# Kernel tuning notes

Hardware: AMD Instinct MI355X
Metric: run time of the kernel (lower is better)

## Reference

```python
import jax, jax.numpy as jnp
import numpy as np

D_EMBED = 1024


def setup_inputs() -> dict:
    key = jax.random.key(0)
    ks = jax.random.split(key, 8)
    B, S, D = 8, 2048, D_EMBED
    scale = 1.0 / np.sqrt(D)
    return {
        "embeddings": jax.random.normal(ks[0], (B, S, D), dtype=jnp.float32),
        "mask": jnp.zeros((B, S, S), dtype=jnp.float32),
        "Wq": jax.random.normal(ks[1], (D, D), dtype=jnp.float32) * scale,
        "bq": jax.random.normal(ks[2], (D,), dtype=jnp.float32) * 0.02,
        "Wk": jax.random.normal(ks[3], (D, D), dtype=jnp.float32) * scale,
        "bk": jax.random.normal(ks[4], (D,), dtype=jnp.float32) * 0.02,
        "Wv": jax.random.normal(ks[5], (D, D), dtype=jnp.float32) * scale,
        "bv": jax.random.normal(ks[6], (D,), dtype=jnp.float32) * 0.02,
    }


def reference(embeddings, mask, Wq, bq, Wk, bk, Wv, bv):
    # torch Linear: y = x @ W.T + b
    q = jnp.einsum('bsd,ed->bse', embeddings, Wq) + bq
    k = jnp.einsum('bsd,ed->bse', embeddings, Wk) + bk
    v = jnp.einsum('bsd,ed->bse', embeddings, Wv) + bv
    scores = jnp.einsum('bqd,bkd->bqk', q, k)
    # NOTE: faithful to source — mask added BEFORE scaling by 1/sqrt(d)
    scores = (scores + mask) * (1.0 / jnp.sqrt(jnp.float32(q.shape[-1])))
    attn = jax.nn.softmax(scores, axis=-1)
    return jnp.einsum('bqk,bkd->bqd', attn, v)
```

## Files before the change

### kernel.cpp

```cpp
#include <hip/hip_runtime.h>


#define B_SZ 8
#define SEQ  2048
#define DIM  1024
#define MROWS (B_SZ * SEQ)

typedef unsigned short u16;
typedef short short8 __attribute__((ext_vector_type(8)));
typedef unsigned short u16x4 __attribute__((ext_vector_type(4)));
typedef float f32x4 __attribute__((ext_vector_type(4)));

__device__ __forceinline__ u16 f2h(float x) {
  _Float16 h = (_Float16)x;
  union { _Float16 f; u16 u; } c; c.f = h; return c.u;
}
__device__ __forceinline__ float h2f(u16 u) {
  union { _Float16 f; u16 u; } c; c.u = u; return (float)c.f;
}

__device__ __forceinline__ int xcd_swz(int x, int nwg) {
  return (x & 7) * (nwg >> 3) + (x >> 3);
}

__device__ __forceinline__ void gload_lds16(const u16* g, u16* l) {
  __builtin_amdgcn_global_load_lds(
      (__attribute__((address_space(1))) void*)(g),
      (__attribute__((address_space(3))) void*)(l), 16, 0, 0);
}

__device__ __forceinline__ f32x4 mfma_f16(short8 a, short8 b, f32x4 c) {
  asm("v_mfma_f32_16x16x32_f16 %0, %1, %2, %0" : "+v"(c) : "v"(a), "v"(b));
  return c;
}

__device__ __forceinline__ void gemm256_core(const u16* __restrict__ Ag,
                                             const u16* __restrict__ Bg,
                                             int NT, size_t lda, size_t ldb,
                                             u16* sm, f32x4 (&acc)[8][4]) {
  const int tid = threadIdx.x;
  const int lane = tid & 63;
  const int wid = tid >> 6;
  const int wm8 = (wid >> 2) << 3;
  const int wn4 = (wid & 3) << 2;

  u16* sA = sm;
  u16* sB = sm + 32768;

  const int bb = (lane << 4) ^ (((lane >> 5) & 1) << 5);
  const int rins = bb >> 6;
  const int cins = (bb & 63) >> 1;
  const int s0 = wid, s1 = 8 + wid, s2 = 16 + wid, s3 = 24 + wid;
  const size_t aoff0 = (size_t)((s0 >> 1) * 16 + rins) * lda + ((s0 & 1) * 32 + cins);
  const size_t aoff1 = (size_t)((s1 >> 1) * 16 + rins) * lda + ((s1 & 1) * 32 + cins);
  const size_t aoff2 = (size_t)((s2 >> 1) * 16 + rins) * lda + ((s2 & 1) * 32 + cins);
  const size_t aoff3 = (size_t)((s3 >> 1) * 16 + rins) * lda + ((s3 & 1) * 32 + cins);
  const size_t boff0 = (size_t)((s0 >> 1) * 16 + rins) * ldb + ((s0 & 1) * 32 + cins);
  const size_t boff1 = (size_t)((s1 >> 1) * 16 + rins) * ldb + ((s1 & 1) * 32 + cins);
  const size_t boff2 = (size_t)((s2 >> 1) * 16 + rins) * ldb + ((s2 & 1) * 32 + cins);
  const size_t boff3 = (size_t)((s3 >> 1) * 16 + rins) * ldb + ((s3 & 1) * 32 + cins);
  const int wid512 = wid << 9;

  const int lof = ((lane & 15) << 6) + ((lane >> 4) << 4);
  const int loe = (lof ^ (((lane >> 3) & 1) << 5)) >> 1;

#define ISSUE_A(j, nb, kt) \
  gload_lds16(Ag + aoff##j + (size_t)(kt) * 64, sA + (nb) * 16384 + (j) * 4096 + wid512)
#define ISSUE_B(j, nb, kt) \
  gload_lds16(Bg + boff##j + (size_t)(kt) * 64, sB + (nb) * 16384 + (j) * 4096 + wid512)

  ISSUE_B(0, 0, 0); ISSUE_B(1, 0, 0); ISSUE_B(2, 0, 0); ISSUE_B(3, 0, 0);
  ISSUE_A(0, 0, 0); ISSUE_A(2, 0, 0); ISSUE_A(1, 0, 0); ISSUE_A(3, 0, 0);

  int buf = 0;
  for (int kt = 0; kt < NT; ++kt) {
    const int nk = kt + 1;
    const bool pre = nk < NT;
    const int nb = buf ^ 1;
    asm volatile("s_waitcnt vmcnt(2)" ::: "memory");
    __builtin_amdgcn_s_barrier();
    asm volatile("" ::: "memory");
    const u16* bufA = sA + buf * 16384;
    const u16* bufB = sB + buf * 16384;
    short8 bf[4][2];
    short8 a0[2][2], a1[2][2];
#pragma unroll
    for (int n = 0; n < 4; ++n) {
      bf[n][0] = *(const short8*)(bufB + (wn4 + n) * 1024 + loe);
      bf[n][1] = *(const short8*)(bufB + (wn4 + n) * 1024 + 512 + loe);
    }
#pragma unroll
    for (int m = 0; m < 2; ++m) {
      a0[m][0] = *(const short8*)(bufA + (wm8 + m) * 1024 + loe);
      a0[m][1] = *(const short8*)(bufA + (wm8 + m) * 1024 + 512 + loe);
    }
    if (pre) { ISSUE_B(0, nb, nk); ISSUE_B(1, nb, nk); }
    __builtin_amdgcn_s_setprio(1);
#pragma unroll
    for (int m = 0; m < 2; ++m)
#pragma unroll
      for (int n = 0; n < 4; ++n) {
        acc[m][n] = mfma_f16(a0[m][0], bf[n][0], acc[m][n]);
        acc[m][n] = mfma_f16(a0[m][1], bf[n][1], acc[m][n]);
      }
    __builtin_amdgcn_s_setprio(0);
#pragma unroll
    for (int m = 0; m < 2; ++m) {
      a1[m][0] = *(const short8*)(bufA + (wm8 + 2 + m) * 1024 + loe);
      a1[m][1] = *(const short8*)(bufA + (wm8 + 2 + m) * 1024 + 512 + loe);
    }
    if (pre) { ISSUE_B(2, nb, nk); ISSUE_B(3, nb, nk); }
    __builtin_amdgcn_s_barrier();
    asm volatile("" ::: "memory");
    __builtin_amdgcn_s_setprio(1);
#pragma unroll
    for (int m = 0; m < 2; ++m)
#pragma unroll
      for (int n = 0; n < 4; ++n) {
        acc[2 + m][n] = mfma_f16(a1[m][0], bf[n][0], acc[2 + m][n]);
        acc[2 + m][n] = mfma_f16(a1[m][1], bf[n][1], acc[2 + m][n]);
      }
    __builtin_amdgcn_s_setprio(0);
    if (pre) {
      asm volatile("s_waitcnt vmcnt(4)" ::: "memory");
    } else {
      asm volatile("s_waitcnt vmcnt(0)" ::: "memory");
    }
    __builtin_amdgcn_s_barrier();
    asm volatile("" ::: "memory");
#pragma unroll
    for (int m = 0; m < 2; ++m) {
      a0[m][0] = *(const short8*)(bufA + (wm8 + 4 + m) * 1024 + loe);
      a0[m][1] = *(const short8*)(bufA + (wm8 + 4 + m) * 1024 + 512 + loe);
      a1[m][0] = *(const short8*)(bufA + (wm8 + 6 + m) * 1024 + loe);
      a1[m][1] = *(const short8*)(bufA + (wm8 + 6 + m) * 1024 + 512 + loe);
    }
    if (pre) { ISSUE_A(0, nb, nk); ISSUE_A(2, nb, nk); }
    __builtin_amdgcn_s_setprio(1);
#pragma unroll
    for (int m = 0; m < 2; ++m)
#pragma unroll
      for (int n = 0; n < 4; ++n) {
        acc[4 + m][n] = mfma_f16(a0[m][0], bf[n][0], acc[4 + m][n]);
        acc[4 + m][n] = mfma_f16(a0[m][1], bf[n][1], acc[4 + m][n]);
      }
    __builtin_amdgcn_s_setprio(0);
    if (pre) { ISSUE_A(1, nb, nk); ISSUE_A(3, nb, nk); }
    __builtin_amdgcn_s_barrier();
    asm volatile("" ::: "memory");
    __builtin_amdgcn_s_setprio(1);
#pragma unroll
    for (int m = 0; m < 2; ++m)
#pragma unroll
      for (int n = 0; n < 4; ++n) {
        acc[6 + m][n] = mfma_f16(a1[m][0], bf[n][0], acc[6 + m][n]);
        acc[6 + m][n] = mfma_f16(a1[m][1], bf[n][1], acc[6 + m][n]);
      }
    __builtin_amdgcn_s_setprio(0);
    buf ^= 1;
  }
  asm volatile("s_nop 7\n\ts_nop 7\n\ts_nop 7" ::);
#undef ISSUE_A
#undef ISSUE_B
}

__device__ __forceinline__ void gemm128_core(const u16* A, const u16* Bt, int K,
                                             int lda, int ldb, f32x4 (&acc)[4][4],
                                             u16* sA, u16* sB) {
  const int tid = threadIdx.x;
  const int lane = tid & 63;
  const int wid = tid >> 6;
  const int wr = wid >> 1;
  const int wc = wid & 1;
  const int srow = tid >> 2;
  const int scol = (tid & 3) << 3;
  const u16* ga0 = A + (size_t)srow * lda + scol;
  const u16* ga1 = A + (size_t)(srow + 64) * lda + scol;
  const u16* gb0 = Bt + (size_t)srow * ldb + scol;
  const u16* gb1 = Bt + (size_t)(srow + 64) * ldb + scol;
  u16* la0 = sA + (wid << 9);
  u16* la1 = sA + 2048 + (wid << 9);
  u16* lb0 = sB + (wid << 9);
  u16* lb1 = sB + 2048 + (wid << 9);
  const u16* pa = sA + (size_t)((wr << 6) + (lane & 15)) * 32 + ((lane >> 4) << 3);
  const u16* pb = sB + (size_t)((wc << 6) + (lane & 15)) * 32 + ((lane >> 4) << 3);
  const int ksteps = K >> 5;
  for (int kt = 0; kt < ksteps; ++kt) {
    gload_lds16(ga0, la0);
    gload_lds16(ga1, la1);
    gload_lds16(gb0, lb0);
    gload_lds16(gb1, lb1);
    ga0 += 32; ga1 += 32; gb0 += 32; gb1 += 32;
    __syncthreads();
    short8 a[4], b[4];
#pragma unroll
    for (int i = 0; i < 4; ++i) a[i] = *(const short8*)(pa + (i << 9));
#pragma unroll
    for (int i = 0; i < 4; ++i) b[i] = *(const short8*)(pb + (i << 9));
#pragma unroll
    for (int mi = 0; mi < 4; ++mi)
#pragma unroll
      for (int ni = 0; ni < 4; ++ni)
        acc[mi][ni] = mfma_f16(a[mi], b[ni], acc[mi][ni]);
    __syncthreads();
  }
  asm volatile("s_nop 7\n\ts_nop 7\n\ts_nop 7" ::);
}

__global__ __launch_bounds__(256) void prep_kernel(const float* __restrict__ emb,
                                                   const float* __restrict__ Wq,
                                                   const float* __restrict__ Wk,
                                                   const float* __restrict__ Wv,
                                                   const float* __restrict__ bq,
                                                   u16* __restrict__ emb16,
                                                   u16* __restrict__ WqT,
                                                   u16* __restrict__ WkT,
                                                   u16* __restrict__ Wv16,
                                                   float* __restrict__ w) {
  __shared__ float t[64][65];
  const int b = blockIdx.x;
  const int tid = threadIdx.x;
  if (b < 16384) {
    int i = b * 256 + tid;
    float4 v = ((const float4*)emb)[i];
    u16x4 o;
    o[0] = f2h(v.x); o[1] = f2h(v.y); o[2] = f2h(v.z); o[3] = f2h(v.w);
    ((u16x4*)emb16)[i] = o;
  } else if (b < 16896) {
    const int b2 = b - 16384;
    const float* src = (b2 >> 8) ? Wk : Wq;
    u16* dst = (b2 >> 8) ? WkT : WqT;
    const int rem = b2 & 255;
    const int r0 = (rem >> 4) * 64;
    const int c0 = (rem & 15) * 64;
    const int tr = tid >> 4;
    const int c4 = (tid & 15) << 2;
#pragma unroll
    for (int i = 0; i < 4; ++i) {
      float4 x = *(const float4*)(src + (size_t)(r0 + tr + 16 * i) * 1024 + c0 + c4);
      t[tr + 16 * i][c4 + 0] = x.x;
      t[tr + 16 * i][c4 + 1] = x.y;
      t[tr + 16 * i][c4 + 2] = x.z;
      t[tr + 16 * i][c4 + 3] = x.w;
    }
    __syncthreads();
#pragma unroll
    for (int i = 0; i < 4; ++i) {
      int dr = tr + 16 * i;
      u16x4 y;
      y[0] = f2h(t[c4 + 0][dr]);
      y[1] = f2h(t[c4 + 1][dr]);
      y[2] = f2h(t[c4 + 2][dr]);
      y[3] = f2h(t[c4 + 3][dr]);
      *(u16x4*)(dst + (size_t)(c0 + dr) * 1024 + r0 + c4) = y;
    }
  } else if (b < 17920) {
    int i = (b - 16896) * 256 + tid;
    float4 v = ((const float4*)Wv)[i];
    u16x4 o;
    o[0] = f2h(v.x); o[1] = f2h(v.y); o[2] = f2h(v.z); o[3] = f2h(v.w);
    ((u16x4*)Wv16)[i] = o;
  } else {
    const int wb = b - 17920;
    const int el = tid & 31;
    const int rg = tid >> 5;
    const int e = wb * 32 + el;
    float s = 0.f;
    const float* col = Wk + e;
#pragma unroll 4
    for (int r = rg * 128; r < rg * 128 + 128; ++r)
      s += col[(size_t)r * 1024] * bq[r];
    float* red = &t[0][0];
    red[rg * 32 + el] = s;
    __syncthreads();
    if (tid < 32) {
      float a = 0.f;
#pragma unroll
      for (int g = 0; g < 8; ++g) a += red[g * 32 + tid];
      w[wb * 32 + tid] = a * 0.03125f;
    }
  }
}

__global__ __launch_bounds__(256) void cmt_kernel(const u16* __restrict__ emb16,
                                                  const u16* __restrict__ WqT,
                                                  const u16* __restrict__ WkT,
                                                  const float* __restrict__ w,
                                                  float* __restrict__ c,
                                                  float* __restrict__ MtP) {
  __shared__ __align__(16) u16 smem[8192];
  const int b = blockIdx.x;
  const int tid = threadIdx.x;
  if (b < 4096) {
    float* sw = (float*)smem;
    for (int i = tid; i < 1024; i += 256) sw[i] = w[i];
    __syncthreads();
    const int wv = tid >> 6, lane = tid & 63;
    const int r = b * 4 + wv;
    const u16* row = emb16 + (size_t)r * 1024;
    float s = 0.f;
#pragma unroll
    for (int it = 0; it < 2; ++it) {
      int d = lane * 8 + it * 512;
      short8 v = *(const short8*)(row + d);
#pragma unroll
      for (int j = 0; j < 8; ++j) s += h2f((u16)v[j]) * sw[d + j];
    }
#pragma unroll
    for (int off = 1; off < 64; off <<= 1) s += __shfl_xor(s, off);
    if (lane == 0) c[r] = s;
  } else {
    const int b2 = b - 4096;
    const int tile = b2 >> 2;
    const int kc = b2 & 3;
    const int m0 = (tile >> 3) * 128;
    const int n0 = (tile & 7) * 128;
    f32x4 acc[4][4] = {};
    gemm128_core(WkT + (size_t)m0 * 1024 + kc * 256,
                 WqT + (size_t)n0 * 1024 + kc * 256, 256, 1024, 1024,
                 acc, smem, smem + 4096);
    const int lane = tid & 63, wid = tid >> 6;
    const int wr = wid >> 1, wc = wid & 1;
    float* plane = MtP + (size_t)kc * 1024 * 1024;
#pragma unroll
    for (int mi = 0; mi < 4; ++mi)
#pragma unroll
      for (int ni = 0; ni < 4; ++ni)
#pragma unroll
        for (int j = 0; j < 4; ++j) {
          int row = m0 + (wr << 6) + mi * 16 + ((lane >> 4) << 2) + j;
          int col = n0 + (wc << 6) + ni * 16 + (lane & 15);
          plane[(size_t)row * 1024 + col] = acc[mi][ni][j];
        }
  }
}

__global__ __launch_bounds__(256) void mtred_kernel(const float* __restrict__ MtP,
                                                    u16* __restrict__ Mt) {
  const size_t i = (size_t)blockIdx.x * 1024 + threadIdx.x * 4;
  float4 a = *(const float4*)(MtP + i);
  float4 b = *(const float4*)(MtP + 1048576 + i);
  float4 cc = *(const float4*)(MtP + 2097152 + i);
  float4 d = *(const float4*)(MtP + 3145728 + i);
  u16x4 o;
  o[0] = f2h((a.x + b.x + cc.x + d.x) * 0.03125f);
  o[1] = f2h((a.y + b.y + cc.y + d.y) * 0.03125f);
  o[2] = f2h((a.z + b.z + cc.z + d.z) * 0.03125f);
  o[3] = f2h((a.w + b.w + cc.w + d.w) * 0.03125f);
  *(u16x4*)(Mt + i) = o;
}

__global__ __launch_bounds__(512) void proj256_kernel(const u16* __restrict__ emb16,
                                                      const u16* __restrict__ Mt,
                                                      const u16* __restrict__ Wv16,
                                                      const float* __restrict__ bv,
                                                      u16* __restrict__ G,
                                                      u16* __restrict__ vT) {
  __shared__ __align__(16) u16 sm[65536];
  const int wg = xcd_swz(blockIdx.x, 512);
  const int lane = threadIdx.x & 63, wid = threadIdx.x >> 6;
  f32x4 acc[8][4] = {};
  if (wg < 256) {
    const int m0 = (wg >> 2) * 256;
    const int n0 = (wg & 3) * 256;
    gemm256_core(emb16 + (size_t)m0 * 1024, Mt + (size_t)n0 * 1024, 16, 1024, 1024,
                 sm, acc);
    const int rb = m0 + ((wid >> 2) << 7) + ((lane >> 4) << 2);
    const int cb = n0 + ((wid & 3) << 6) + (lane & 15);
#pragma unroll
    for (int m = 0; m < 8; ++m)
#pragma unroll
      for (int n = 0; n < 4; ++n)
#pragma unroll
        for (int j = 0; j < 4; ++j)
          G[(size_t)(rb + m * 16 + j) * 1024 + (cb + n * 16)] = f2h(acc[m][n][j]);
  } else {
    const int r = wg - 256;
    const int m0 = (r & 3) * 256;
    const int n0 = (r >> 2) * 256;
    gemm256_core(Wv16 + (size_t)m0 * 1024, emb16 + (size_t)n0 * 1024, 16, 1024, 1024,
                 sm, acc);
    const int rb = m0 + ((wid >> 2) << 7) + ((lane >> 4) << 2);
    const int cb = n0 + ((wid & 3) << 6) + (lane & 15);
#pragma unroll
    for (int m = 0; m < 8; ++m)
#pragma unroll
      for (int n = 0; n < 4; ++n)
#pragma unroll
        for (int j = 0; j < 4; ++j) {
          int d = rb + m * 16 + j;
          int kg = cb + n * 16;
          int bi = kg >> 11, s = kg & 2047;
          vT[((size_t)bi << 21) + ((size_t)d << 11) + s] = f2h(acc[m][n][j] + bv[d]);
        }
  }
}

__global__ __launch_bounds__(512) void scores256_kernel(const u16* __restrict__ G,
                                                        const u16* __restrict__ emb16,
                                                        const float* __restrict__ c,
                                                        u16* __restrict__ scH) {
  __shared__ __align__(16) u16 sm[65536];
  const int wg = xcd_swz(blockIdx.x, 512);
  const int b = wg >> 6;
  const int m0 = ((wg >> 3) & 7) * 256;
  const int n0 = (wg & 7) * 256;
  f32x4 acc[8][4] = {};
  gemm256_core(G + ((size_t)b * SEQ + m0) * DIM, emb16 + ((size_t)b * SEQ + n0) * DIM,
               16, DIM, DIM, sm, acc);
  const int lane = threadIdx.x & 63, wid = threadIdx.x >> 6;
  const int rb = m0 + ((wid >> 2) << 7) + ((lane >> 4) << 2);
  const int cb = n0 + ((wid & 3) << 6) + (lane & 15);
  float cn[4];
#pragma unroll
  for (int n = 0; n < 4; ++n) cn[n] = c[(size_t)b * SEQ + cb + n * 16];
#pragma unroll
  for (int m = 0; m < 8; ++m)
#pragma unroll
    for (int n = 0; n < 4; ++n)
#pragma unroll
      for (int j = 0; j < 4; ++j) {
        size_t idx = ((size_t)b * SEQ + rb + m * 16 + j) * SEQ + (cb + n * 16);
        scH[idx] = f2h(acc[m][n][j] + cn[n]);
      }
}

__global__ __launch_bounds__(256) void softmax_kernel(u16* __restrict__ scH,
                                                      const float* __restrict__ mask) {
  __shared__ float red[8];
  const size_t row = blockIdx.x;
  u16* rowp = scH + row * SEQ;
  const float* mrow = mask + row * SEQ;
  const int tid = threadIdx.x;
  short8 raw = *(const short8*)(rowp + tid * 8);
  float4 m0 = ((const float4*)mrow)[2 * tid];
  float4 m1 = ((const float4*)mrow)[2 * tid + 1];
  float mk[8] = {m0.x, m0.y, m0.z, m0.w, m1.x, m1.y, m1.z, m1.w};
  float f[8];
#pragma unroll
  for (int j = 0; j < 8; ++j) f[j] = h2f((u16)raw[j]) + mk[j] * 0.03125f;
  float mx = f[0];
#pragma unroll
  for (int j = 1; j < 8; ++j) mx = fmaxf(mx, f[j]);
#pragma unroll
  for (int off = 1; off < 64; off <<= 1) mx = fmaxf(mx, __shfl_xor(mx, off));
  const int wid = tid >> 6, lane = tid & 63;
  if (lane == 0) red[wid] = mx;
  __syncthreads();
  mx = fmaxf(fmaxf(red[0], red[1]), fmaxf(red[2], red[3]));
  float e[8];
  float s = 0.f;
#pragma unroll
  for (int j = 0; j < 8; ++j) {
    e[j] = __expf(f[j] - mx);
    s += e[j];
  }
#pragma unroll
  for (int off = 1; off < 64; off <<= 1) s += __shfl_xor(s, off);
  if (lane == 0) red[4 + wid] = s;
  __syncthreads();
  s = (red[4] + red[5]) + (red[6] + red[7]);
  const float inv = 1.f / s;
  short8 o;
#pragma unroll
  for (int j = 0; j < 8; ++j) o[j] = (short)f2h(e[j] * inv);
  *(short8*)(rowp + tid * 8) = o;
}

__global__ __launch_bounds__(512) void pv256_kernel(const u16* __restrict__ pr,
                                                    const u16* __restrict__ vt,
                                                    float* __restrict__ out) {
  __shared__ __align__(16) u16 sm[65536];
  const int wg = xcd_swz(blockIdx.x, 256);
  const int b = wg >> 5;
  const int m0 = ((wg >> 2) & 7) * 256;
  const int n0 = (wg & 3) * 256;
  f32x4 acc[8][4] = {};
  gemm256_core(pr + ((size_t)b * SEQ + m0) * SEQ, vt + ((size_t)b * DIM + n0) * SEQ,
               32, SEQ, SEQ, sm, acc);
  const int lane = threadIdx.x & 63, wid = threadIdx.x >> 6;
  const int rb = m0 + ((wid >> 2) << 7) + ((lane >> 4) << 2);
  const int cb = n0 + ((wid & 3) << 6) + (lane & 15);
#pragma unroll
  for (int m = 0; m < 8; ++m)
#pragma unroll
    for (int n = 0; n < 4; ++n)
#pragma unroll
      for (int j = 0; j < 4; ++j)
        out[((size_t)b * SEQ + rb + m * 16 + j) * DIM + (cb + n * 16)] = acc[m][n][j];
}

extern "C" void kernel_launch(void* const* d_in, const int* in_sizes, int n_in,
                              void* d_out, int out_size, void* d_ws, size_t ws_size,
                              hipStream_t stream) {
  const float* emb  = (const float*)d_in[0];
  const float* mask = (const float*)d_in[1];
  const float* Wq   = (const float*)d_in[2];
  const float* bq   = (const float*)d_in[3];
  const float* Wk   = (const float*)d_in[4];
  const float* bk   = (const float*)d_in[5];
  const float* Wv   = (const float*)d_in[6];
  const float* bv   = (const float*)d_in[7];
  float* out = (float*)d_out;
  (void)bk;

  const size_t M1 = 1024 * 1024;
  u16* scH   = (u16*)d_ws;
  u16* emb16 = scH + 32 * M1;
  u16* WqT   = emb16 + 16 * M1;
  u16* WkT   = WqT + M1;
  u16* Wv16  = WkT + M1;
  u16* Mt    = Wv16 + M1;
  u16* G     = Mt + M1;
  u16* vT    = G + 16 * M1;
  float* MtP = (float*)(vT + 16 * M1);
  float* w   = MtP + 4 * M1;
  float* c   = w + 1024;

  prep_kernel<<<17952, 256, 0, stream>>>(emb, Wq, Wk, Wv, bq, emb16, WqT, WkT, Wv16, w);
  cmt_kernel<<<4352, 256, 0, stream>>>(emb16, WqT, WkT, w, c, MtP);
  mtred_kernel<<<1024, 256, 0, stream>>>(MtP, Mt);

  proj256_kernel<<<512, 512, 0, stream>>>(emb16, Mt, Wv16, bv, G, vT);

  scores256_kernel<<<512, 512, 0, stream>>>(G, emb16, c, scH);
  softmax_kernel<<<MROWS, 256, 0, stream>>>(scH, mask);
  pv256_kernel<<<256, 512, 0, stream>>>((const u16*)scH, vT, out);
}
```

Measured before the change: 297.3 us.

## Double waves per block in 256x256 GEMM core with new LDS swizzle

Reworks the shared 256x256 GEMM core to use 16 waves (1024 threads) per block, each computing a 64x64 sub-tile instead of 128x64. LDS staging uses a new row/k-chunk XOR swizzle with four 16-byte async loads per thread per tile, and the per-k-tile schedule is cut from four barrier phases to two halves of 32 k. This aims to raise latency hiding and cut per-wave register pressure from accumulators. The trade-off is more LDS fragment reads per MFMA and more barrier participants.

```diff
diff --git a/kernel.cpp b/kernel.cpp
--- a/kernel.cpp
+++ b/kernel.cpp
@@ -37,90 +37,61 @@
 __device__ __forceinline__ void gemm256_core(const u16* __restrict__ Ag,
                                              const u16* __restrict__ Bg,
                                              int NT, size_t lda, size_t ldb,
-                                             u16* sm, f32x4 (&acc)[8][4]) {
+                                             u16* sm, f32x4 (&acc)[4][4]) {
   const int tid = threadIdx.x;
   const int lane = tid & 63;
   const int wid = tid >> 6;
-  const int wm8 = (wid >> 2) << 3;
-  const int wn4 = (wid & 3) << 2;
+  const int wm = wid >> 2;
+  const int wn = wid & 3;
 
   u16* sA = sm;
   u16* sB = sm + 32768;
 
-  const int bb = (lane << 4) ^ (((lane >> 5) & 1) << 5);
-  const int rins = bb >> 6;
-  const int cins = (bb & 63) >> 1;
-  const int s0 = wid, s1 = 8 + wid, s2 = 16 + wid, s3 = 24 + wid;
-  const size_t aoff0 = (size_t)((s0 >> 1) * 16 + rins) * lda + ((s0 & 1) * 32 + cins);
-  const size_t aoff1 = (size_t)((s1 >> 1) * 16 + rins) * lda + ((s1 & 1) * 32 + cins);
-  const size_t aoff2 = (size_t)((s2 >> 1) * 16 + rins) * lda + ((s2 & 1) * 32 + cins);
-  const size_t aoff3 = (size_t)((s3 >> 1) * 16 + rins) * lda + ((s3 & 1) * 32 + cins);
-  const size_t boff0 = (size_t)((s0 >> 1) * 16 + rins) * ldb + ((s0 & 1) * 32 + cins);
-  const size_t boff1 = (size_t)((s1 >> 1) * 16 + rins) * ldb + ((s1 & 1) * 32 + cins);
-  const size_t boff2 = (size_t)((s2 >> 1) * 16 + rins) * ldb + ((s2 & 1) * 32 + cins);
-  const size_t boff3 = (size_t)((s3 >> 1) * 16 + rins) * ldb + ((s3 & 1) * 32 + cins);
-  const int wid512 = wid << 9;
-
-  const int lof = ((lane & 15) << 6) + ((lane >> 4) << 4);
-  const int loe = (lof ^ (((lane >> 3) & 1) << 5)) >> 1;
-
-#define ISSUE_A(j, nb, kt) \
-  gload_lds16(Ag + aoff##j + (size_t)(kt) * 64, sA + (nb) * 16384 + (j) * 4096 + wid512)
-#define ISSUE_B(j, nb, kt) \
-  gload_lds16(Bg + boff##j + (size_t)(kt) * 64, sB + (nb) * 16384 + (j) * 4096 + wid512)
-
-  ISSUE_B(0, 0, 0); ISSUE_B(1, 0, 0); ISSUE_B(2, 0, 0); ISSUE_B(3, 0, 0);
-  ISSUE_A(0, 0, 0); ISSUE_A(2, 0, 0); ISSUE_A(1, 0, 0); ISSUE_A(3, 0, 0);
+  const int r_s = tid >> 2;
+  const int ko_s = (tid & 3) ^ ((tid >> 3) & 3);
+  const size_t aoffs = (size_t)r_s * lda + ko_s * 8;
+  const size_t boffs = (size_t)r_s * ldb + ko_s * 8;
+  const int wdst = wid << 9;
+
+  const int lof = ((lane & 15) << 5) + ((((lane >> 4) ^ ((lane >> 1) & 3))) << 3);
+  const int abase = (wm << 11) + lof;
+  const int bbase = (wn << 11) + lof;
+
+#define ISSUE_TILE(nb, kt)                                                        \
+  do {                                                                            \
+    gload_lds16(Bg + boffs + (size_t)(kt) * 64,      sB + (nb) * 16384 + wdst);   \
+    gload_lds16(Ag + aoffs + (size_t)(kt) * 64,      sA + (nb) * 16384 + wdst);   \
+    gload_lds16(Bg + boffs + (size_t)(kt) * 64 + 32, sB + (nb) * 16384 + 8192 + wdst); \
+    gload_lds16(Ag + aoffs + (size_t)(kt) * 64 + 32, sA + (nb) * 16384 + 8192 + wdst); \
+  } while (0)
+
+  ISSUE_TILE(0, 0);
 
   int buf = 0;
   for (int kt = 0; kt < NT; ++kt) {
-    const int nk = kt + 1;
-    const bool pre = nk < NT;
+    const bool pre = (kt + 1) < NT;
     const int nb = buf ^ 1;
     asm volatile("s_waitcnt vmcnt(2)" ::: "memory");
     __builtin_amdgcn_s_barrier();
     asm volatile("" ::: "memory");
     const u16* bufA = sA + buf * 16384;
     const u16* bufB = sB + buf * 16384;
-    short8 bf[4][2];
-    short8 a0[2][2], a1[2][2];
-#pragma unroll
-    for (int n = 0; n < 4; ++n) {
-      bf[n][0] = *(const short8*)(bufB + (wn4 + n) * 1024 + loe);
-      bf[n][1] = *(const short8*)(bufB + (wn4 + n) * 1024 + 512 + loe);
-    }
-#pragma unroll
-    for (int m = 0; m < 2; ++m) {
-      a0[m][0] = *(const short8*)(bufA + (wm8 + m) * 1024 + loe);
-      a0[m][1] = *(const short8*)(bufA + (wm8 + m) * 1024 + 512 + loe);
-    }
-    if (pre) { ISSUE_B(0, nb, nk); ISSUE_B(1, nb, nk); }
-    __builtin_amdgcn_s_setprio(1);
-#pragma unroll
-    for (int m = 0; m < 2; ++m)
-#pragma unroll
-      for (int n = 0; n < 4; ++n) {
-        acc[m][n] = mfma_f16(a0[m][0], bf[n][0], acc[m][n]);
-        acc[m][n] = mfma_f16(a0[m][1], bf[n][1], acc[m][n]);
+    {
+      short8 bf[4];
+#pragma unroll
+      for (int n = 0; n < 4; ++n)
+        bf[n] = *(const short8*)(bufB + bbase + (n << 9));
+      if (pre) ISSUE_TILE(nb, kt + 1);
+      __builtin_amdgcn_s_setprio(1);
+#pragma unroll
+      for (int m = 0; m < 4; ++m) {
+        short8 af = *(const short8*)(bufA + abase + (m << 9));
+#pragma unroll
+        for (int n = 0; n < 4; ++n)
+          acc[m][n] = mfma_f16(af, bf[n], acc[m][n]);
       }
-    __builtin_amdgcn_s_setprio(0);
-#pragma unroll
-    for (int m = 0; m < 2; ++m) {
-      a1[m][0] = *(const short8*)(bufA + (wm8 + 2 + m) * 1024 + loe);
-      a1[m][1] = *(const short8*)(bufA + (wm8 + 2 + m) * 1024 + 512 + loe);
-    }
-    if (pre) { ISSUE_B(2, nb, nk); ISSUE_B(3, nb, nk); }
-    __builtin_amdgcn_s_barrier();
-    asm volatile("" ::: "memory");
-    __builtin_amdgcn_s_setprio(1);
-#pragma unroll
-    for (int m = 0; m < 2; ++m)
-#pragma unroll
-      for (int n = 0; n < 4; ++n) {
-        acc[2 + m][n] = mfma_f16(a1[m][0], bf[n][0], acc[2 + m][n]);
-        acc[2 + m][n] = mfma_f16(a1[m][1], bf[n][1], acc[2 + m][n]);
-      }
-    __builtin_amdgcn_s_setprio(0);
+      __builtin_amdgcn_s_setprio(0);
+    }
     if (pre) {
       asm volatile("s_waitcnt vmcnt(4)" ::: "memory");
     } else {
@@ -128,40 +99,25 @@
     }
     __builtin_amdgcn_s_barrier();
     asm volatile("" ::: "memory");
-#pragma unroll
-    for (int m = 0; m < 2; ++m) {
-      a0[m][0] = *(const short8*)(bufA + (wm8 + 4 + m) * 1024 + loe);
-      a0[m][1] = *(const short8*)(bufA + (wm8 + 4 + m) * 1024 + 512 + loe);
-      a1[m][0] = *(const short8*)(bufA + (wm8 + 6 + m) * 1024 + loe);
-      a1[m][1] = *(const short8*)(bufA + (wm8 + 6 + m) * 1024 + 512 + loe);
-    }
-    if (pre) { ISSUE_A(0, nb, nk); ISSUE_A(2, nb, nk); }
-    __builtin_amdgcn_s_setprio(1);
-#pragma unroll
-    for (int m = 0; m < 2; ++m)
-#pragma unroll
-      for (int n = 0; n < 4; ++n) {
-        acc[4 + m][n] = mfma_f16(a0[m][0], bf[n][0], acc[4 + m][n]);
-        acc[4 + m][n] = mfma_f16(a0[m][1], bf[n][1], acc[4 + m][n]);
+    {
+      short8 bf[4];
+#pragma unroll
+      for (int n = 0; n < 4; ++n)
+        bf[n] = *(const short8*)(bufB + 8192 + bbase + (n << 9));
+      __builtin_amdgcn_s_setprio(1);
+#pragma unroll
+      for (int m = 0; m < 4; ++m) {
+        short8 af = *(const short8*)(bufA + 8192 + abase + (m << 9));
+#pragma unroll
+        for (int n = 0; n < 4; ++n)
+          acc[m][n] = mfma_f16(af, bf[n], acc[m][n]);
       }
-    __builtin_amdgcn_s_setprio(0);
-    if (pre) { ISSUE_A(1, nb, nk); ISSUE_A(3, nb, nk); }
-    __builtin_amdgcn_s_barrier();
-    asm volatile("" ::: "memory");
-    __builtin_amdgcn_s_setprio(1);
-#pragma unroll
-    for (int m = 0; m < 2; ++m)
-#pragma unroll
-      for (int n = 0; n < 4; ++n) {
-        acc[6 + m][n] = mfma_f16(a1[m][0], bf[n][0], acc[6 + m][n]);
-        acc[6 + m][n] = mfma_f16(a1[m][1], bf[n][1], acc[6 + m][n]);
-      }
-    __builtin_amdgcn_s_setprio(0);
+      __builtin_amdgcn_s_setprio(0);
+    }
     buf ^= 1;
   }
   asm volatile("s_nop 7\n\ts_nop 7\n\ts_nop 7" ::);
-#undef ISSUE_A
-#undef ISSUE_B
+#undef ISSUE_TILE
 }
 
 __device__ __forceinline__ void gemm128_core(const u16* A, const u16* Bt, int K,
@@ -350,25 +306,27 @@
   *(u16x4*)(Mt + i) = o;
 }
 
-__global__ __launch_bounds__(512) void proj256_kernel(const u16* __restrict__ emb16,
-                                                      const u16* __restrict__ Mt,
-                                                      const u16* __restrict__ Wv16,
-                                                      const float* __restrict__ bv,
-                                                      u16* __restrict__ G,
-                                                      u16* __restrict__ vT) {
+__global__ __launch_bounds__(1024) void proj256_kernel(const u16* __restrict__ emb16,
+                                                       const u16* __restrict__ Mt,
+                                                       const u16* __restrict__ Wv16,
+                                                       const float* __restrict__ bv,
+                                                       u16* __restrict__ G,
+                                                       u16* __restrict__ vT) {
   __shared__ __align__(16) u16 sm[65536];
   const int wg = xcd_swz(blockIdx.x, 512);
   const int lane = threadIdx.x & 63, wid = threadIdx.x >> 6;
-  f32x4 acc[8][4] = {};
+  f32x4 acc[4][4] = {};
+  const int rbw = ((wid >> 2) << 6) + ((lane >> 4) << 2);
+  const int cbw = ((wid & 3) << 6) + (lane & 15);
   if (wg < 256) {
     const int m0 = (wg >> 2) * 256;
     const int n0 = (wg & 3) * 256;
     gemm256_core(emb16 + (size_t)m0 * 1024, Mt + (size_t)n0 * 1024, 16, 1024, 1024,
                  sm, acc);
-    const int rb = m0 + ((wid >> 2) << 7) + ((lane >> 4) << 2);
-    const int cb = n0 + ((wid & 3) << 6) + (lane & 15);
-#pragma unroll
-    for (int m = 0; m < 8; ++m)
+    const int rb = m0 + rbw;
+    const int cb = n0 + cbw;
+#pragma unroll
+    for (int m = 0; m < 4; ++m)
 #pragma unroll
       for (int n = 0; n < 4; ++n)
 #pragma unroll
@@ -380,10 +338,10 @@
     const int n0 = (r >> 2) * 256;
     gemm256_core(Wv16 + (size_t)m0 * 1024, emb16 + (size_t)n0 * 1024, 16, 1024, 1024,
                  sm, acc);
-    const int rb = m0 + ((wid >> 2) << 7) + ((lane >> 4) << 2);
-    const int cb = n0 + ((wid & 3) << 6) + (lane & 15);
-#pragma unroll
-    for (int m = 0; m < 8; ++m)
+    const int rb = m0 + rbw;
+    const int cb = n0 + cbw;
+#pragma unroll
+    for (int m = 0; m < 4; ++m)
 #pragma unroll
       for (int n = 0; n < 4; ++n)
 #pragma unroll
@@ -396,26 +354,26 @@
   }
 }
 
-__global__ __launch_bounds__(512) void scores256_kernel(const u16* __restrict__ G,
-                                                        const u16* __restrict__ emb16,
-                                                        const float* __restrict__ c,
-                                                        u16* __restrict__ scH) {
+__global__ __launch_bounds__(1024) void scores256_kernel(const u16* __restrict__ G,
+                                                         const u16* __restrict__ emb16,
+                                                         const float* __restrict__ c,
+                                                         u16* __restrict__ scH) {
   __shared__ __align__(16) u16 sm[65536];
   const int wg = xcd_swz(blockIdx.x, 512);
   const int b = wg >> 6;
   const int m0 = ((wg >> 3) & 7) * 256;
   const int n0 = (wg & 7) * 256;
-  f32x4 acc[8][4] = {};
+  f32x4 acc[4][4] = {};
   gemm256_core(G + ((size_t)b * SEQ + m0) * DIM, emb16 + ((size_t)b * SEQ + n0) * DIM,
                16, DIM, DIM, sm, acc);
   const int lane = threadIdx.x & 63, wid = threadIdx.x >> 6;
-  const int rb = m0 + ((wid >> 2) << 7) + ((lane >> 4) << 2);
+  const int rb = m0 + ((wid >> 2) << 6) + ((lane >> 4) << 2);
   const int cb = n0 + ((wid & 3) << 6) + (lane & 15);
   float cn[4];
 #pragma unroll
   for (int n = 0; n < 4; ++n) cn[n] = c[(size_t)b * SEQ + cb + n * 16];
 #pragma unroll
-  for (int m = 0; m < 8; ++m)
+  for (int m = 0; m < 4; ++m)
 #pragma unroll
     for (int n = 0; n < 4; ++n)
 #pragma unroll
@@ -467,22 +425,22 @@
   *(short8*)(rowp + tid * 8) = o;
 }
 
-__global__ __launch_bounds__(512) void pv256_kernel(const u16* __restrict__ pr,
-                                                    const u16* __restrict__ vt,
-                                                    float* __restrict__ out) {
+__global__ __launch_bounds__(1024) void pv256_kernel(const u16* __restrict__ pr,
+                                                     const u16* __restrict__ vt,
+                                                     float* __restrict__ out) {
   __shared__ __align__(16) u16 sm[65536];
   const int wg = xcd_swz(blockIdx.x, 256);
   const int b = wg >> 5;
   const int m0 = ((wg >> 2) & 7) * 256;
   const int n0 = (wg & 3) * 256;
-  f32x4 acc[8][4] = {};
+  f32x4 acc[4][4] = {};
   gemm256_core(pr + ((size_t)b * SEQ + m0) * SEQ, vt + ((size_t)b * DIM + n0) * SEQ,
                32, SEQ, SEQ, sm, acc);
   const int lane = threadIdx.x & 63, wid = threadIdx.x >> 6;
-  const int rb = m0 + ((wid >> 2) << 7) + ((lane >> 4) << 2);
+  const int rb = m0 + ((wid >> 2) << 6) + ((lane >> 4) << 2);
   const int cb = n0 + ((wid & 3) << 6) + (lane & 15);
 #pragma unroll
-  for (int m = 0; m < 8; ++m)
+  for (int m = 0; m < 4; ++m)
 #pragma unroll
     for (int n = 0; n < 4; ++n)
 #pragma unroll
@@ -521,9 +479,9 @@
   cmt_kernel<<<4352, 256, 0, stream>>>(emb16, WqT, WkT, w, c, MtP);
   mtred_kernel<<<1024, 256, 0, stream>>>(MtP, Mt);
 
-  proj256_kernel<<<512, 512, 0, stream>>>(emb16, Mt, Wv16, bv, G, vT);
-
-  scores256_kernel<<<512, 512, 0, stream>>>(G, emb16, c, scH);
+  proj256_kernel<<<512, 1024, 0, stream>>>(emb16, Mt, Wv16, bv, G, vT);
+
+  scores256_kernel<<<512, 1024, 0, stream>>>(G, emb16, c, scH);
   softmax_kernel<<<MROWS, 256, 0, stream>>>(scH, mask);
-  pv256_kernel<<<256, 512, 0, stream>>>((const u16*)scH, vT, out);
-}
+  pv256_kernel<<<256, 1024, 0, stream>>>((const u16*)scH, vT, out);
+}
```

Measured after the change: 315.7 us. +6.2%, slower.
